# Kernel tuning notes

Hardware: AMD Instinct MI355X
Metric: run time of the kernel (lower is better)

Reference implementation:

```python
import jax, jax.numpy as jnp
import numpy as np

NUM_STEPS = 8
THRESHOLD = 0.5


def _glorot(key, shape):
    fan_in = shape[0]
    return jax.random.normal(key, shape, dtype=jnp.float32) / np.sqrt(fan_in).astype(np.float32)


def setup_inputs() -> dict:
    key = jax.random.key(0)
    ks = jax.random.split(key, 24)
    B, APM = 2048, 32           # molecules, atoms per molecule
    N = B * APM                 # 65536 nodes
    E = N * 4                   # 262144 directed edges
    NF, EF, NH, EH, MA = 64, 16, 128, 128, 256
    inp = {}
    inp['mol_a_reprs'] = jax.random.normal(ks[0], (B, MA), dtype=jnp.float32)
    inp['node_features'] = jax.random.normal(ks[1], (N, NF), dtype=jnp.float32)
    inp['edge_features'] = jax.random.normal(ks[2], (E, EF), dtype=jnp.float32)
    inp['node_hidden0'] = jnp.zeros((N, NH), dtype=jnp.float32)
    inp['edge_hidden0'] = jnp.zeros((E, EH), dtype=jnp.float32)
    inp['edges'] = jax.random.randint(ks[3], (2, E), 0, N, dtype=jnp.int32)
    inp['batch_indices'] = jnp.repeat(jnp.arange(B, dtype=jnp.int32), APM)  # sorted, in-range
    # MPN weights (no bias)
    inp['W1'] = _glorot(ks[4], (NF, EH))   # src node features -> edge hidden
    inp['W2'] = _glorot(ks[5], (EF, EH))   # edge features -> edge hidden
    inp['W3'] = _glorot(ks[6], (NH, EH))   # src node hidden -> edge hidden
    inp['U1'] = _glorot(ks[7], (NF, NH))   # node features -> node hidden
    inp['U2'] = _glorot(ks[8], (EH, NH))   # aggregated edge hidden -> node hidden
    # pick-atom MLP: (MA+NH)->256->128->64->1
    inp['M1w'] = _glorot(ks[9], (MA + NH, 256)); inp['M1b'] = jnp.zeros((256,), jnp.float32)
    inp['M2w'] = _glorot(ks[10], (256, 128));    inp['M2b'] = jnp.zeros((128,), jnp.float32)
    inp['M3w'] = _glorot(ks[11], (128, 64));     inp['M3b'] = jnp.zeros((64,), jnp.float32)
    inp['M4w'] = _glorot(ks[12], (64, 1));       inp['M4b'] = jnp.zeros((1,), jnp.float32)
    return inp


def _mpn(node_features, edge_features, node_h, edge_h, src, dst, W1, W2, W3, U1, U2):
    N = node_features.shape[0]
    W1x_src = node_features[src] @ W1          # [E, EH], loop-invariant
    W2e = edge_features @ W2                   # [E, EH], loop-invariant
    U1x = node_features @ U1                   # [N, NH], loop-invariant
    for _ in range(NUM_STEPS):
        agg = jax.ops.segment_sum(edge_h, dst, num_segments=N)   # [N, EH]
        node_h = jax.nn.relu(U1x + agg @ U2)                     # [N, NH]
        edge_h = jax.nn.relu(W1x_src + W2e + node_h[src] @ W3)   # [E, EH]
    return node_h


def reference(mol_a_reprs, node_features, edge_features, node_hidden0, edge_hidden0,
              edges, batch_indices, W1, W2, W3, U1, U2,
              M1w, M1b, M2w, M2b, M3w, M3b, M4w, M4b):
    src, dst = edges[0], edges[1]
    node_h = _mpn(node_features, edge_features, node_hidden0, edge_hidden0,
                  src, dst, W1, W2, W3, U1, U2)
    b_atom_mol_a = mol_a_reprs[batch_indices]                    # index_select gather [N, MA]
    x = jnp.concatenate([node_h, b_atom_mol_a], axis=1)          # [N, NH+MA]
    x = jax.nn.relu(x @ M1w + M1b)
    x = jax.nn.relu(x @ M2w + M2b)
    x = jax.nn.relu(x @ M3w + M3b)
    p = jax.nn.sigmoid(x @ M4w + M4b)                            # [N, 1]
    return p >= THRESHOLD
```

## Files before the change

kernel.cpp:

```cpp
#include <hip/hip_runtime.h>
#include <cstddef>

#define NF 64
#define EF 16
#define NH 128
#define EH 128
#define MA 256

static inline int ceil_div(int a, int b) { return (a + b - 1) / b; }

__global__ __launch_bounds__(256) void gemm64_kernel(
    const float* __restrict__ A, const float* __restrict__ Bw,
    float* __restrict__ C,
    const float* __restrict__ addR, const int* __restrict__ addIdx,
    const float* __restrict__ bias,
    int M, int K, int Nc, int doRelu, int reluA)
{
    __shared__ float As[16][68];
    __shared__ float Bs[16][132];
    const int tid = threadIdx.x;
    const int tx = tid & 15;
    const int ty = tid >> 4;
    const int m0 = blockIdx.y << 6;
    const int n0 = blockIdx.x << 7;

    const int lr = tid >> 2;
    const int lc = (tid & 3) << 2;
    const int br = tid >> 4;
    const int bc = (tid & 15) << 3;

    float acc[4][8];
#pragma unroll
    for (int i = 0; i < 4; ++i)
#pragma unroll
        for (int j = 0; j < 8; ++j) acc[i][j] = 0.0f;

    const float* aptr = A + (size_t)(m0 + lr) * K + lc;

    for (int k0 = 0; k0 < K; k0 += 16) {
        float4 a4 = *(const float4*)(aptr + k0);
        float4 b0 = *(const float4*)(Bw + (size_t)(k0 + br) * Nc + n0 + bc);
        float4 b1 = *(const float4*)(Bw + (size_t)(k0 + br) * Nc + n0 + bc + 4);
        if (reluA) {
            a4.x = fmaxf(a4.x, 0.f); a4.y = fmaxf(a4.y, 0.f);
            a4.z = fmaxf(a4.z, 0.f); a4.w = fmaxf(a4.w, 0.f);
        }
        __syncthreads();
        As[lc + 0][lr] = a4.x; As[lc + 1][lr] = a4.y;
        As[lc + 2][lr] = a4.z; As[lc + 3][lr] = a4.w;
        *(float4*)&Bs[br][bc] = b0;
        *(float4*)&Bs[br][bc + 4] = b1;
        __syncthreads();
#pragma unroll
        for (int kk = 0; kk < 16; ++kk) {
            float4 av = *(const float4*)&As[kk][ty * 4];
            float4 bv0 = *(const float4*)&Bs[kk][tx * 8];
            float4 bv1 = *(const float4*)&Bs[kk][tx * 8 + 4];
            float a[4] = {av.x, av.y, av.z, av.w};
            float b[8] = {bv0.x, bv0.y, bv0.z, bv0.w, bv1.x, bv1.y, bv1.z, bv1.w};
#pragma unroll
            for (int i = 0; i < 4; ++i)
#pragma unroll
                for (int j = 0; j < 8; ++j)
                    acc[i][j] = fmaf(a[i], b[j], acc[i][j]);
        }
    }

    const int c = n0 + tx * 8;
    float4 bvl = make_float4(0.f, 0.f, 0.f, 0.f), bvh = bvl;
    if (bias) { bvl = *(const float4*)(bias + c); bvh = *(const float4*)(bias + c + 4); }
#pragma unroll
    for (int i = 0; i < 4; ++i) {
        int r = m0 + ty * 4 + i;
        float4 vl = make_float4(acc[i][0], acc[i][1], acc[i][2], acc[i][3]);
        float4 vh = make_float4(acc[i][4], acc[i][5], acc[i][6], acc[i][7]);
        if (addR) {
            int ar = addIdx ? addIdx[r] : r;
            float4 al = *(const float4*)(addR + (size_t)ar * Nc + c);
            float4 ah = *(const float4*)(addR + (size_t)ar * Nc + c + 4);
            vl.x += al.x; vl.y += al.y; vl.z += al.z; vl.w += al.w;
            vh.x += ah.x; vh.y += ah.y; vh.z += ah.z; vh.w += ah.w;
        }
        vl.x += bvl.x; vl.y += bvl.y; vl.z += bvl.z; vl.w += bvl.w;
        vh.x += bvh.x; vh.y += bvh.y; vh.z += bvh.z; vh.w += bvh.w;
        if (doRelu) {
            vl.x = fmaxf(vl.x, 0.f); vl.y = fmaxf(vl.y, 0.f); vl.z = fmaxf(vl.z, 0.f); vl.w = fmaxf(vl.w, 0.f);
            vh.x = fmaxf(vh.x, 0.f); vh.y = fmaxf(vh.y, 0.f); vh.z = fmaxf(vh.z, 0.f); vh.w = fmaxf(vh.w, 0.f);
        }
        *(float4*)(C + (size_t)r * Nc + c) = vl;
        *(float4*)(C + (size_t)r * Nc + c + 4) = vh;
    }
}

__global__ __launch_bounds__(256) void hist_kernel(const int* __restrict__ dst, int* __restrict__ deg, int E) {
    int e = blockIdx.x * 256 + threadIdx.x;
    if (e < E) atomicAdd(&deg[dst[e]], 1);
}

__global__ __launch_bounds__(256) void scan_block_kernel(const int* __restrict__ deg, int* __restrict__ rp,
                                                         int* __restrict__ bsum) {
    __shared__ int buf[256];
    int tid = threadIdx.x;
    int i = blockIdx.x * 256 + tid;
    int v = deg[i];
    buf[tid] = v;
    __syncthreads();
    for (int off = 1; off < 256; off <<= 1) {
        int t = (tid >= off) ? buf[tid - off] : 0;
        __syncthreads();
        buf[tid] += t;
        __syncthreads();
    }
    rp[i] = buf[tid] - v;
    if (tid == 255) bsum[blockIdx.x] = buf[255];
}

__global__ __launch_bounds__(256) void scan_top_kernel(const int* __restrict__ bsum, int* __restrict__ boff,
                                                       int* __restrict__ rp, int N) {
    __shared__ int buf[256];
    int tid = threadIdx.x;
    int v = bsum[tid];
    buf[tid] = v;
    __syncthreads();
    for (int off = 1; off < 256; off <<= 1) {
        int t = (tid >= off) ? buf[tid - off] : 0;
        __syncthreads();
        buf[tid] += t;
        __syncthreads();
    }
    boff[tid] = buf[tid] - v;
    if (tid == 255) rp[N] = buf[255];
}

__global__ __launch_bounds__(256) void scan_add_kernel(int* __restrict__ rp, int* __restrict__ cursor,
                                                       const int* __restrict__ boff) {
    int tid = threadIdx.x;
    int i = blockIdx.x * 256 + tid;
    int v = rp[i] + boff[blockIdx.x];
    rp[i] = v;
    cursor[i] = v;
}

__global__ __launch_bounds__(256) void scatter_kernel(const int* __restrict__ dst, const int* __restrict__ src,
                                                      int* __restrict__ cursor,
                                                      int* __restrict__ eid, int* __restrict__ srcS, int E) {
    int e = blockIdx.x * 256 + threadIdx.x;
    if (e < E) {
        int p = atomicAdd(&cursor[dst[e]], 1);
        eid[p] = e;
        srcS[p] = src[e];
    }
}

__global__ __launch_bounds__(256) void gather_ef_kernel(const float* __restrict__ ef, const int* __restrict__ eid,
                                                        float* __restrict__ efS, int E) {
    int idx = blockIdx.x * 256 + threadIdx.x;
    int p = idx >> 2, comp = idx & 3;
    if (p < E) {
        int e = eid[p];
        float4 v = *(const float4*)(ef + (size_t)e * EF + comp * 4);
        *(float4*)(efS + (size_t)p * EF + comp * 4) = v;
    }
}

__global__ __launch_bounds__(256) void agg_kernel(const float* __restrict__ nodeT, const float* __restrict__ efS,
                                                  const int* __restrict__ rp, const int* __restrict__ srcS,
                                                  const float* __restrict__ W2, float* __restrict__ agg) {
    const int n = blockIdx.x * 8 + threadIdx.y;
    const int c = threadIdx.x << 2;
    float4 w2r[16];
#pragma unroll
    for (int k = 0; k < 16; ++k) w2r[k] = *(const float4*)(W2 + (size_t)k * EH + c);

    const int p0 = rp[n], p1 = rp[n + 1];
    float4 s = make_float4(0.f, 0.f, 0.f, 0.f);
    for (int p = p0; p < p1; ++p) {
        const int sn = srcS[p];
        const float* ep = efS + (size_t)p * EF;
        float4 e0 = *(const float4*)(ep);
        float4 e1 = *(const float4*)(ep + 4);
        float4 e2 = *(const float4*)(ep + 8);
        float4 e3 = *(const float4*)(ep + 12);
        float ef16[16] = {e0.x, e0.y, e0.z, e0.w, e1.x, e1.y, e1.z, e1.w,
                          e2.x, e2.y, e2.z, e2.w, e3.x, e3.y, e3.z, e3.w};
        float4 w = make_float4(0.f, 0.f, 0.f, 0.f);
#pragma unroll
        for (int k = 0; k < 16; ++k) {
            w.x = fmaf(ef16[k], w2r[k].x, w.x);
            w.y = fmaf(ef16[k], w2r[k].y, w.y);
            w.z = fmaf(ef16[k], w2r[k].z, w.z);
            w.w = fmaf(ef16[k], w2r[k].w, w.w);
        }
        float4 t = *(const float4*)(nodeT + (size_t)sn * EH + c);
        s.x += fmaxf(t.x + w.x, 0.f);
        s.y += fmaxf(t.y + w.y, 0.f);
        s.z += fmaxf(t.z + w.z, 0.f);
        s.w += fmaxf(t.w + w.w, 0.f);
    }
    *(float4*)(agg + (size_t)n * EH + c) = s;
}

__global__ __launch_bounds__(256) void x3final_kernel(const float* __restrict__ x2, const float* __restrict__ M3w,
                                                      const float* __restrict__ b3, const float* __restrict__ M4w,
                                                      const float* __restrict__ b4, int* __restrict__ out) {
    __shared__ float As[16][132];
    __shared__ float Bs[16][68];
    __shared__ float red[128][17];
    const int tid = threadIdx.x;
    const int tx = tid & 15;
    const int ty = tid >> 4;
    const int m0 = blockIdx.x << 7;
    const int lr = tid >> 1, lc = (tid & 1) << 3;
    const int br = tid >> 4, bc = (tid & 15) << 2;

    float acc[8][4];
#pragma unroll
    for (int i = 0; i < 8; ++i)
#pragma unroll
        for (int j = 0; j < 4; ++j) acc[i][j] = 0.0f;

    const float* aptr = x2 + (size_t)(m0 + lr) * 128 + lc;
    for (int k0 = 0; k0 < 128; k0 += 16) {
        float4 a0 = *(const float4*)(aptr + k0);
        float4 a1 = *(const float4*)(aptr + k0 + 4);
        float4 bv = *(const float4*)(M3w + (size_t)(k0 + br) * 64 + bc);
        __syncthreads();
        As[lc + 0][lr] = a0.x; As[lc + 1][lr] = a0.y; As[lc + 2][lr] = a0.z; As[lc + 3][lr] = a0.w;
        As[lc + 4][lr] = a1.x; As[lc + 5][lr] = a1.y; As[lc + 6][lr] = a1.z; As[lc + 7][lr] = a1.w;
        *(float4*)&Bs[br][bc] = bv;
        __syncthreads();
#pragma unroll
        for (int kk = 0; kk < 16; ++kk) {
            float4 av0 = *(const float4*)&As[kk][ty * 8];
            float4 av1 = *(const float4*)&As[kk][ty * 8 + 4];
            float4 bv0 = *(const float4*)&Bs[kk][tx * 4];
            float a[8] = {av0.x, av0.y, av0.z, av0.w, av1.x, av1.y, av1.z, av1.w};
            float b[4] = {bv0.x, bv0.y, bv0.z, bv0.w};
#pragma unroll
            for (int i = 0; i < 8; ++i)
#pragma unroll
                for (int j = 0; j < 4; ++j)
                    acc[i][j] = fmaf(a[i], b[j], acc[i][j]);
        }
    }

    const int c = tx * 4;
    float4 b3v = *(const float4*)(b3 + c);
    float4 w4v = *(const float4*)(M4w + c);
#pragma unroll
    for (int i = 0; i < 8; ++i) {
        float p = fmaxf(acc[i][0] + b3v.x, 0.f) * w4v.x
                + fmaxf(acc[i][1] + b3v.y, 0.f) * w4v.y
                + fmaxf(acc[i][2] + b3v.z, 0.f) * w4v.z
                + fmaxf(acc[i][3] + b3v.w, 0.f) * w4v.w;
        red[ty * 8 + i][tx] = p;
    }
    __syncthreads();
    if (tid < 128) {
        float z = b4[0];
#pragma unroll
        for (int j = 0; j < 16; ++j) z += red[tid][j];
        out[m0 + tid] = z >= 0.f ? 1 : 0;
    }
}

extern "C" void kernel_launch(void* const* d_in, const int* in_sizes, int n_in,
                              void* d_out, int out_size, void* d_ws, size_t ws_size,
                              hipStream_t stream)
{
    const float* mol_a = (const float*)d_in[0];
    const float* nf    = (const float*)d_in[1];
    const float* ef    = (const float*)d_in[2];
    const int*   edges = (const int*)d_in[5];
    const int*   batch = (const int*)d_in[6];
    const float* W1  = (const float*)d_in[7];
    const float* W2  = (const float*)d_in[8];
    const float* W3  = (const float*)d_in[9];
    const float* U1  = (const float*)d_in[10];
    const float* U2  = (const float*)d_in[11];
    const float* M1w = (const float*)d_in[12];
    const float* M1b = (const float*)d_in[13];
    const float* M2w = (const float*)d_in[14];
    const float* M2b = (const float*)d_in[15];
    const float* M3w = (const float*)d_in[16];
    const float* M3b = (const float*)d_in[17];
    const float* M4w = (const float*)d_in[18];
    const float* M4b = (const float*)d_in[19];

    const int N = in_sizes[3] / NH;
    const int E = in_sizes[4] / EH;
    const int B = in_sizes[0] / MA;
    const int* srcp = edges;
    const int* dstp = edges + E;

    char* ws = (char*)d_ws;
    size_t off = 0;
    auto alloc = [&](size_t bytes) -> char* {
        char* p = ws + off;
        off = (off + bytes + 255) & ~(size_t)255;
        return p;
    };
    int* deg     = (int*)alloc((size_t)N * 4);
    int* rp      = (int*)alloc(((size_t)N + 1) * 4);
    int* cursor  = (int*)alloc((size_t)N * 4);
    int* bsum    = (int*)alloc(256 * 4);
    int* boff    = (int*)alloc(256 * 4);
    int* eid     = (int*)alloc((size_t)E * 4);
    int* srcS    = (int*)alloc((size_t)E * 4);
    float* efS     = (float*)alloc((size_t)E * EF * 4);
    float* nodePre = (float*)alloc((size_t)N * EH * 4);
    float* U1x     = (float*)alloc((size_t)N * NH * 4);
    float* node_h  = (float*)alloc((size_t)N * NH * 4);
    float* nodeTa  = (float*)alloc((size_t)N * EH * 4);
    float* nodeTb  = (float*)alloc((size_t)N * EH * 4);
    float* aggp    = (float*)alloc((size_t)N * EH * 4);
    float* molPart = (float*)alloc((size_t)B * 256 * 4);
    float* x1      = (float*)alloc((size_t)N * 256 * 4);
    float* x2 = nodeTa;

    hipMemsetAsync(deg, 0, (size_t)N * 4, stream);
    hist_kernel<<<ceil_div(E, 256), 256, 0, stream>>>(dstp, deg, E);
    scan_block_kernel<<<N / 256, 256, 0, stream>>>(deg, rp, bsum);
    scan_top_kernel<<<1, 256, 0, stream>>>(bsum, boff, rp, N);
    scan_add_kernel<<<N / 256, 256, 0, stream>>>(rp, cursor, boff);
    scatter_kernel<<<ceil_div(E, 256), 256, 0, stream>>>(dstp, srcp, cursor, eid, srcS, E);
    gather_ef_kernel<<<ceil_div(E * 4, 256), 256, 0, stream>>>(ef, eid, efS, E);

    gemm64_kernel<<<dim3(1, N / 64), 256, 0, stream>>>(nf, W1, nodePre, nullptr, nullptr, nullptr, N, NF, EH, 0, 0);
    gemm64_kernel<<<dim3(1, N / 64), 256, 0, stream>>>(nf, U1, U1x, nullptr, nullptr, nullptr, N, NF, NH, 0, 0);

    gemm64_kernel<<<dim3(1, N / 64), 256, 0, stream>>>(U1x, W3, nodeTa, nodePre, nullptr, nullptr, N, NH, EH, 0, 1);

    float* curT = nodeTa;
    float* nxtT = nodeTb;
    for (int s = 0; s < 6; ++s) {
        agg_kernel<<<N / 8, dim3(32, 8), 0, stream>>>(curT, efS, rp, srcS, W2, aggp);
        gemm64_kernel<<<dim3(1, N / 64), 256, 0, stream>>>(aggp, U2, node_h, U1x, nullptr, nullptr, N, EH, NH, 1, 0);
        gemm64_kernel<<<dim3(1, N / 64), 256, 0, stream>>>(node_h, W3, nxtT, nodePre, nullptr, nullptr, N, NH, EH, 0, 0);
        float* t = curT; curT = nxtT; nxtT = t;
    }
    agg_kernel<<<N / 8, dim3(32, 8), 0, stream>>>(curT, efS, rp, srcS, W2, aggp);
    gemm64_kernel<<<dim3(1, N / 64), 256, 0, stream>>>(aggp, U2, node_h, U1x, nullptr, nullptr, N, EH, NH, 1, 0);

    gemm64_kernel<<<dim3(2, B / 64), 256, 0, stream>>>(mol_a, M1w + 128 * 256, molPart, nullptr, nullptr, M1b, B, MA, 256, 0, 0);
    gemm64_kernel<<<dim3(2, N / 64), 256, 0, stream>>>(node_h, M1w, x1, molPart, batch, nullptr, N, NH, 256, 1, 0);
    gemm64_kernel<<<dim3(1, N / 64), 256, 0, stream>>>(x1, M2w, x2, nullptr, nullptr, M2b, N, 256, 128, 1, 0);
    x3final_kernel<<<N / 128, 256, 0, stream>>>(x2, M3w, M3b, M4w, M4b, (int*)d_out);
}
```

Measured before the change: 1.258 ms.

## Stage full-K A tiles in LDS, read B from global, fuse edge-feature gather into scatter

The GEMM kernel now loads up to 128 K-columns of the A tile into dynamic shared memory in one pass and reads the small weight matrix B directly from global memory (cache-resident), instead of double-staging 16-wide K slices with two barriers per slice. This cuts barrier count and LDS traffic for B, at the cost of more LDS per block (up to ~35KB), which may lower occupancy, and uncoalesced-per-k global B reads that rely on cache. Separately, the edge-feature permutation is folded into the scatter kernel, dropping the eid buffer and one launch. The molecule-part GEMM is also moved earlier in the launch order.

```diff
diff --git a/kernel.cpp b/kernel.cpp
--- a/kernel.cpp
+++ b/kernel.cpp
@@ -9,55 +9,54 @@
 
 static inline int ceil_div(int a, int b) { return (a + b - 1) / b; }
 
-__global__ __launch_bounds__(256) void gemm64_kernel(
+__global__ __launch_bounds__(256) void gemmB_kernel(
     const float* __restrict__ A, const float* __restrict__ Bw,
     float* __restrict__ C,
     const float* __restrict__ addR, const int* __restrict__ addIdx,
     const float* __restrict__ bias,
     int M, int K, int Nc, int doRelu, int reluA)
 {
-    __shared__ float As[16][68];
-    __shared__ float Bs[16][132];
+    extern __shared__ float As[];
     const int tid = threadIdx.x;
     const int tx = tid & 15;
     const int ty = tid >> 4;
     const int m0 = blockIdx.y << 6;
     const int n0 = blockIdx.x << 7;
 
-    const int lr = tid >> 2;
-    const int lc = (tid & 3) << 2;
-    const int br = tid >> 4;
-    const int bc = (tid & 15) << 3;
-
     float acc[4][8];
 #pragma unroll
     for (int i = 0; i < 4; ++i)
 #pragma unroll
         for (int j = 0; j < 8; ++j) acc[i][j] = 0.0f;
 
-    const float* aptr = A + (size_t)(m0 + lr) * K + lc;
-
-    for (int k0 = 0; k0 < K; k0 += 16) {
-        float4 a4 = *(const float4*)(aptr + k0);
-        float4 b0 = *(const float4*)(Bw + (size_t)(k0 + br) * Nc + n0 + bc);
-        float4 b1 = *(const float4*)(Bw + (size_t)(k0 + br) * Nc + n0 + bc + 4);
-        if (reluA) {
-            a4.x = fmaxf(a4.x, 0.f); a4.y = fmaxf(a4.y, 0.f);
-            a4.z = fmaxf(a4.z, 0.f); a4.w = fmaxf(a4.w, 0.f);
-        }
-        __syncthreads();
-        As[lc + 0][lr] = a4.x; As[lc + 1][lr] = a4.y;
-        As[lc + 2][lr] = a4.z; As[lc + 3][lr] = a4.w;
-        *(float4*)&Bs[br][bc] = b0;
-        *(float4*)&Bs[br][bc + 4] = b1;
-        __syncthreads();
-#pragma unroll
-        for (int kk = 0; kk < 16; ++kk) {
-            float4 av = *(const float4*)&As[kk][ty * 4];
-            float4 bv0 = *(const float4*)&Bs[kk][tx * 8];
-            float4 bv1 = *(const float4*)&Bs[kk][tx * 8 + 4];
+    for (int kc = 0; kc < K; kc += 128) {
+        const int KC = (K - kc < 128) ? (K - kc) : 128;
+        if (kc) __syncthreads();
+        const int ksh = (KC == 128) ? 5 : 4;
+        const int kmask = (1 << ksh) - 1;
+        for (int idx = tid; idx < (64 << ksh); idx += 256) {
+            const int row = idx >> ksh;
+            const int kq = (idx & kmask) << 2;
+            float4 a4 = *(const float4*)(A + (size_t)(m0 + row) * K + kc + kq);
+            if (reluA) {
+                a4.x = fmaxf(a4.x, 0.f); a4.y = fmaxf(a4.y, 0.f);
+                a4.z = fmaxf(a4.z, 0.f); a4.w = fmaxf(a4.w, 0.f);
+            }
+            As[(kq + 0) * 68 + row] = a4.x;
+            As[(kq + 1) * 68 + row] = a4.y;
+            As[(kq + 2) * 68 + row] = a4.z;
+            As[(kq + 3) * 68 + row] = a4.w;
+        }
+        __syncthreads();
+
+        const float* bbase = Bw + (size_t)kc * Nc + n0 + tx * 8;
+#pragma unroll 4
+        for (int k = 0; k < KC; ++k) {
+            float4 av = *(const float4*)&As[k * 68 + ty * 4];
+            float4 b0 = *(const float4*)(bbase + (size_t)k * Nc);
+            float4 b1 = *(const float4*)(bbase + (size_t)k * Nc + 4);
             float a[4] = {av.x, av.y, av.z, av.w};
-            float b[8] = {bv0.x, bv0.y, bv0.z, bv0.w, bv1.x, bv1.y, bv1.z, bv1.w};
+            float b[8] = {b0.x, b0.y, b0.z, b0.w, b1.x, b1.y, b1.z, b1.w};
 #pragma unroll
             for (int i = 0; i < 4; ++i)
 #pragma unroll
@@ -142,24 +141,15 @@
 }
 
 __global__ __launch_bounds__(256) void scatter_kernel(const int* __restrict__ dst, const int* __restrict__ src,
-                                                      int* __restrict__ cursor,
-                                                      int* __restrict__ eid, int* __restrict__ srcS, int E) {
+                                                      const float* __restrict__ ef, int* __restrict__ cursor,
+                                                      int* __restrict__ srcS, float* __restrict__ efS, int E) {
     int e = blockIdx.x * 256 + threadIdx.x;
     if (e < E) {
         int p = atomicAdd(&cursor[dst[e]], 1);
-        eid[p] = e;
         srcS[p] = src[e];
-    }
-}
-
-__global__ __launch_bounds__(256) void gather_ef_kernel(const float* __restrict__ ef, const int* __restrict__ eid,
-                                                        float* __restrict__ efS, int E) {
-    int idx = blockIdx.x * 256 + threadIdx.x;
-    int p = idx >> 2, comp = idx & 3;
-    if (p < E) {
-        int e = eid[p];
-        float4 v = *(const float4*)(ef + (size_t)e * EF + comp * 4);
-        *(float4*)(efS + (size_t)p * EF + comp * 4) = v;
+        const float4* efr = (const float4*)(ef + (size_t)e * EF);
+        float4* eo = (float4*)(efS + (size_t)p * EF);
+        eo[0] = efr[0]; eo[1] = efr[1]; eo[2] = efr[2]; eo[3] = efr[3];
     }
 }
 
@@ -305,7 +295,6 @@
     int* cursor  = (int*)alloc((size_t)N * 4);
     int* bsum    = (int*)alloc(256 * 4);
     int* boff    = (int*)alloc(256 * 4);
-    int* eid     = (int*)alloc((size_t)E * 4);
     int* srcS    = (int*)alloc((size_t)E * 4);
     float* efS     = (float*)alloc((size_t)E * EF * 4);
     float* nodePre = (float*)alloc((size_t)N * EH * 4);
@@ -318,32 +307,34 @@
     float* x1      = (float*)alloc((size_t)N * 256 * 4);
     float* x2 = nodeTa;
 
+    const int LDS64  = 64 * 68 * 4;
+    const int LDS128 = 128 * 68 * 4;
+
     hipMemsetAsync(deg, 0, (size_t)N * 4, stream);
     hist_kernel<<<ceil_div(E, 256), 256, 0, stream>>>(dstp, deg, E);
     scan_block_kernel<<<N / 256, 256, 0, stream>>>(deg, rp, bsum);
     scan_top_kernel<<<1, 256, 0, stream>>>(bsum, boff, rp, N);
     scan_add_kernel<<<N / 256, 256, 0, stream>>>(rp, cursor, boff);
-    scatter_kernel<<<ceil_div(E, 256), 256, 0, stream>>>(dstp, srcp, cursor, eid, srcS, E);
-    gather_ef_kernel<<<ceil_div(E * 4, 256), 256, 0, stream>>>(ef, eid, efS, E);
-
-    gemm64_kernel<<<dim3(1, N / 64), 256, 0, stream>>>(nf, W1, nodePre, nullptr, nullptr, nullptr, N, NF, EH, 0, 0);
-    gemm64_kernel<<<dim3(1, N / 64), 256, 0, stream>>>(nf, U1, U1x, nullptr, nullptr, nullptr, N, NF, NH, 0, 0);
-
-    gemm64_kernel<<<dim3(1, N / 64), 256, 0, stream>>>(U1x, W3, nodeTa, nodePre, nullptr, nullptr, N, NH, EH, 0, 1);
+    scatter_kernel<<<ceil_div(E, 256), 256, 0, stream>>>(dstp, srcp, ef, cursor, srcS, efS, E);
+
+    gemmB_kernel<<<dim3(1, N / 64), 256, LDS64, stream>>>(nf, W1, nodePre, nullptr, nullptr, nullptr, N, NF, EH, 0, 0);
+    gemmB_kernel<<<dim3(1, N / 64), 256, LDS64, stream>>>(nf, U1, U1x, nullptr, nullptr, nullptr, N, NF, NH, 0, 0);
+    gemmB_kernel<<<dim3(2, B / 64), 256, LDS128, stream>>>(mol_a, M1w + 128 * 256, molPart, nullptr, nullptr, M1b, B, MA, 256, 0, 0);
+
+    gemmB_kernel<<<dim3(1, N / 64), 256, LDS128, stream>>>(U1x, W3, nodeTa, nodePre, nullptr, nullptr, N, NH, EH, 0, 1);
 
     float* curT = nodeTa;
     float* nxtT = nodeTb;
     for (int s = 0; s < 6; ++s) {
         agg_kernel<<<N / 8, dim3(32, 8), 0, stream>>>(curT, efS, rp, srcS, W2, aggp);
-        gemm64_kernel<<<dim3(1, N / 64), 256, 0, stream>>>(aggp, U2, node_h, U1x, nullptr, nullptr, N, EH, NH, 1, 0);
-        gemm64_kernel<<<dim3(1, N / 64), 256, 0, stream>>>(node_h, W3, nxtT, nodePre, nullptr, nullptr, N, NH, EH, 0, 0);
+        gemmB_kernel<<<dim3(1, N / 64), 256, LDS128, stream>>>(aggp, U2, node_h, U1x, nullptr, nullptr, N, EH, NH, 1, 0);
+        gemmB_kernel<<<dim3(1, N / 64), 256, LDS128, stream>>>(node_h, W3, nxtT, nodePre, nullptr, nullptr, N, NH, EH, 0, 0);
         float* t = curT; curT = nxtT; nxtT = t;
     }
     agg_kernel<<<N / 8, dim3(32, 8), 0, stream>>>(curT, efS, rp, srcS, W2, aggp);
-    gemm64_kernel<<<dim3(1, N / 64), 256, 0, stream>>>(aggp, U2, node_h, U1x, nullptr, nullptr, N, EH, NH, 1, 0);
-
-    gemm64_kernel<<<dim3(2, B / 64), 256, 0, stream>>>(mol_a, M1w + 128 * 256, molPart, nullptr, nullptr, M1b, B, MA, 256, 0, 0);
-    gemm64_kernel<<<dim3(2, N / 64), 256, 0, stream>>>(node_h, M1w, x1, molPart, batch, nullptr, N, NH, 256, 1, 0);
-    gemm64_kernel<<<dim3(1, N / 64), 256, 0, stream>>>(x1, M2w, x2, nullptr, nullptr, M2b, N, 256, 128, 1, 0);
+    gemmB_kernel<<<dim3(1, N / 64), 256, LDS128, stream>>>(aggp, U2, node_h, U1x, nullptr, nullptr, N, EH, NH, 1, 0);
+
+    gemmB_kernel<<<dim3(2, N / 64), 256, LDS128, stream>>>(node_h, M1w, x1, molPart, batch, nullptr, N, NH, 256, 1, 0);
+    gemmB_kernel<<<dim3(1, N / 64), 256, LDS128, stream>>>(x1, M2w, x2, nullptr, nullptr, M2b, N, 256, 128, 1, 0);
     x3final_kernel<<<N / 128, 256, 0, stream>>>(x2, M3w, M3b, M4w, M4b, (int*)d_out);
 }
```

New measurement: 1.721 ms. 36.8% more time.
